# Performance work log

Measured on AMD Instinct MI355X. Metric: run time of the kernel, lower is better.

Reference implementation:

```python
import jax, jax.numpy as jnp
import numpy as np

EMB = 256
HEADS = 2
IMG = 224
P1, P2 = 16, 8
LN_EPS = 1e-5


def _layer_norm(t, g, b):
    m = jnp.mean(t, axis=-1, keepdims=True)
    v = jnp.mean((t - m) ** 2, axis=-1, keepdims=True)
    return (t - m) * jax.lax.rsqrt(v + LN_EPS) * g + b


def _patch_embed(x, W, b, cls_tok, p):
    B, C, H, Wd = x.shape
    h, w = H // p, Wd // p
    # b c (h p1)(w p2) -> b (h w) (p1 p2 c)
    t = x.reshape(B, C, h, p, w, p).transpose(0, 2, 4, 3, 5, 1).reshape(B, h * w, p * p * C)
    t = t @ W + b
    cls = jnp.broadcast_to(cls_tok, (B, 1, cls_tok.shape[-1]))
    return jnp.concatenate([cls, t], axis=1)


def setup_inputs() -> dict:
    key = jax.random.key(0)
    ks = jax.random.split(key, 16)
    s = 0.02
    d = {
        "x": jax.random.normal(ks[0], (128, 3, IMG, IMG), dtype=jnp.float32),
        "W1": jax.random.normal(ks[1], (P1 * P1 * 3, EMB), dtype=jnp.float32) * s,
        "b1": jnp.zeros((EMB,), jnp.float32),
        "cls1": jax.random.normal(ks[2], (1, 1, EMB), dtype=jnp.float32),
        "W2": jax.random.normal(ks[3], (P2 * P2 * 3, EMB), dtype=jnp.float32) * s,
        "b2": jnp.zeros((EMB,), jnp.float32),
        "cls2": jax.random.normal(ks[4], (1, 1, EMB), dtype=jnp.float32),
        "ln1_g": jnp.ones((EMB,), jnp.float32),
        "ln1_b": jnp.zeros((EMB,), jnp.float32),
        "Wq": jax.random.normal(ks[5], (EMB, EMB), dtype=jnp.float32) * s,
        "bq": jnp.zeros((EMB,), jnp.float32),
        "Wk": jax.random.normal(ks[6], (EMB, EMB), dtype=jnp.float32) * s,
        "bk": jnp.zeros((EMB,), jnp.float32),
        "Wv": jax.random.normal(ks[7], (EMB, EMB), dtype=jnp.float32) * s,
        "bv": jnp.zeros((EMB,), jnp.float32),
        "Wp": jax.random.normal(ks[8], (EMB, EMB), dtype=jnp.float32) * s,
        "bp": jnp.zeros((EMB,), jnp.float32),
        "ln2_g": jnp.ones((EMB,), jnp.float32),
        "ln2_b": jnp.zeros((EMB,), jnp.float32),
        "lnc_g": jnp.ones((EMB,), jnp.float32),
        "lnc_b": jnp.zeros((EMB,), jnp.float32),
        "Wc": jax.random.normal(ks[9], (EMB, 2), dtype=jnp.float32) * s,
        "bc": jnp.zeros((2,), jnp.float32),
    }
    return d


def reference(x, W1, b1, cls1, W2, b2, cls2, ln1_g, ln1_b, Wq, bq, Wk, bk, Wv, bv,
              Wp, bp, ln2_g, ln2_b, lnc_g, lnc_b, Wc, bc):
    B = x.shape[0]
    p1 = _patch_embed(x, W1, b1, cls1, P1)   # [B, 197, 256]
    p2 = _patch_embed(x, W2, b2, cls2, P2)   # [B, 785, 256]
    n = p1.shape[1]
    idx = jnp.linspace(0.0, p2.shape[1] - 1, n).astype(jnp.int32)  # truncation like .long()
    p2r = p2[:, idx, :]
    z = jnp.concatenate([p2r, p1], axis=1)   # [B, 394, 256]
    N = z.shape[1]

    h = _layer_norm(z, ln1_g, ln1_b)
    dh = EMB // HEADS
    q = (h @ Wq + bq).reshape(B, N, HEADS, dh).transpose(0, 2, 1, 3)
    k = (h @ Wk + bk).reshape(B, N, HEADS, dh).transpose(0, 2, 1, 3)
    v = (h @ Wv + bv).reshape(B, N, HEADS, dh).transpose(0, 2, 1, 3)
    attn = jnp.einsum('bhqd,bhkd->bhqk', q, k)
    # NOTE: faithful to source — softmax of UNscaled logits, then divide by sqrt(emb)
    attn = jax.nn.softmax(attn, axis=-1) / (EMB ** 0.5)
    o = jnp.einsum('bhqk,bhkd->bhqd', attn, v).transpose(0, 2, 1, 3).reshape(B, N, EMB)
    o = o @ Wp + bp
    o = _layer_norm(o, ln2_g, ln2_b)
    z = z + o

    pooled = jnp.mean(z, axis=1)
    logits = _layer_norm(pooled, lnc_g, lnc_b) @ Wc + bc
    return jax.nn.log_softmax(logits, axis=1)
```

## Files before the change

kernel.cpp:

```cpp
#include <hip/hip_runtime.h>

typedef short short8 __attribute__((ext_vector_type(8)));
typedef float f32x4 __attribute__((ext_vector_type(4)));
typedef unsigned short us4 __attribute__((ext_vector_type(4)));
typedef unsigned short u16;

#define MFMA(a,b,c) __builtin_amdgcn_mfma_f32_16x16x32_bf16((a),(b),(c),0,0,0)

__device__ __forceinline__ u16 f2b(float f) {
    union { float f; unsigned int i; } v; v.f = f;
    unsigned int x = v.i;
    return (u16)((x + 0x7fffu + ((x >> 16) & 1u)) >> 16);
}

__device__ __forceinline__ unsigned int pk2(float lo, float hi) {
    return (unsigned int)f2b(lo) | ((unsigned int)f2b(hi) << 16);
}

__global__ __launch_bounds__(256) void k_wtrans(const float* __restrict__ W1,
        const float* __restrict__ W2, const float* __restrict__ Wq, const float* __restrict__ Wk,
        const float* __restrict__ Wv, const float* __restrict__ Wp,
        u16* __restrict__ w1t, u16* __restrict__ w2t, u16* __restrict__ wqt,
        u16* __restrict__ wkt, u16* __restrict__ wvt, u16* __restrict__ wpt) {
    int bx = blockIdx.x, n = threadIdx.x;
    if (bx < 768) {
        int k = bx, c = k % 3, t = k / 3, pj = t & 15, pi = t >> 4;
        int kp2 = c*256 + pi*16 + pj;
        w1t[(size_t)(kp2 >> 5)*8192 + n*32 + (kp2 & 31)] = f2b(W1[(size_t)k*256 + n]);
    } else if (bx < 960) {
        int k = bx - 768, c = k % 3, t = k / 3, pj = t & 7, pi = t >> 3;
        int kp2 = c*64 + pi*8 + pj;
        w2t[(size_t)(kp2 >> 5)*8192 + n*32 + (kp2 & 31)] = f2b(W2[(size_t)k*256 + n]);
    } else if (bx < 1216) { int k = bx - 960;  wqt[(size_t)(k>>5)*8192 + n*32 + (k&31)] = f2b(Wq[(size_t)k*256 + n]); }
    else if (bx < 1472)   { int k = bx - 1216; wkt[(size_t)(k>>5)*8192 + n*32 + (k&31)] = f2b(Wk[(size_t)k*256 + n]); }
    else if (bx < 1728)   { int k = bx - 1472; wvt[(size_t)(k>>5)*8192 + n*32 + (k&31)] = f2b(Wv[(size_t)k*256 + n]); }
    else                  { int k = bx - 1728; wpt[(size_t)(k>>5)*8192 + n*32 + (k&31)] = f2b(Wp[(size_t)k*256 + n]); }
}

__global__ __launch_bounds__(256) void k_cls(const float* __restrict__ cls1,
        const float* __restrict__ cls2, const float* __restrict__ g1, const float* __restrict__ be1,
        float* __restrict__ z, u16* __restrict__ h) {
    __shared__ float red[16];
    int b = blockIdx.x, e = threadIdx.x, lane = e & 63, w = e >> 6;
    float v0 = cls2[e], v1 = cls1[e];
    z[((size_t)b*394 + 0)*256 + e]   = v0;
    z[((size_t)b*394 + 197)*256 + e] = v1;
    float s0 = v0, q0 = v0*v0, s1 = v1, q1 = v1*v1;
    #pragma unroll
    for (int m = 1; m < 64; m <<= 1) {
        s0 += __shfl_xor(s0, m); q0 += __shfl_xor(q0, m);
        s1 += __shfl_xor(s1, m); q1 += __shfl_xor(q1, m);
    }
    if (lane == 0) { red[w] = s0; red[4+w] = q0; red[8+w] = s1; red[12+w] = q1; }
    __syncthreads();
    float S0 = red[0]+red[1]+red[2]+red[3],   Q0 = red[4]+red[5]+red[6]+red[7];
    float S1 = red[8]+red[9]+red[10]+red[11], Q1 = red[12]+red[13]+red[14]+red[15];
    float m0 = S0*(1.f/256.f), r0 = rsqrtf(Q0*(1.f/256.f) - m0*m0 + 1e-5f);
    float m1 = S1*(1.f/256.f), r1 = rsqrtf(Q1*(1.f/256.f) - m1*m1 + 1e-5f);
    h[((size_t)b*394 + 0)*256 + e]   = f2b((v0-m0)*r0*g1[e] + be1[e]);
    h[((size_t)b*394 + 197)*256 + e] = f2b((v1-m1)*r1*g1[e] + be1[e]);
}

__global__ __launch_bounds__(256) void k_embed1(const float* __restrict__ x,
        const u16* __restrict__ w1t, const float* __restrict__ b1,
        const float* __restrict__ g1, const float* __restrict__ be1,
        float* __restrict__ z, u16* __restrict__ h) {
    __shared__ __align__(16) u16 A[16*776];
    __shared__ __align__(16) u16 Wst[8192];
    __shared__ __align__(16) float S[16*260];
    int b = blockIdx.y, g = blockIdx.x, tid = threadIdx.x;
    int p = tid >> 4, pi = tid & 15;
    int j = g*16 + p;
    uint4 wr0 = *(const uint4*)&w1t[tid*8];
    uint4 wr1 = *(const uint4*)&w1t[2048 + tid*8];
    uint4 wr2 = *(const uint4*)&w1t[4096 + tid*8];
    uint4 wr3 = *(const uint4*)&w1t[6144 + tid*8];
    auto stage = [&](const u16* base, int chunk) {
        __syncthreads();
        *(uint4*)&Wst[tid*8] = wr0;
        *(uint4*)&Wst[2048 + tid*8] = wr1;
        *(uint4*)&Wst[4096 + tid*8] = wr2;
        *(uint4*)&Wst[6144 + tid*8] = wr3;
        __syncthreads();
        if (base) {
            const u16* src = base + (size_t)chunk*8192;
            wr0 = *(const uint4*)&src[tid*8];
            wr1 = *(const uint4*)&src[2048 + tid*8];
            wr2 = *(const uint4*)&src[4096 + tid*8];
            wr3 = *(const uint4*)&src[6144 + tid*8];
        }
    };
    if (j < 196) {
        int hi = j / 14, wi = j - hi*14;
        #pragma unroll
        for (int c = 0; c < 3; ++c) {
            const float* src = x + (((size_t)b*3 + c)*224 + hi*16 + pi)*224 + wi*16;
            #pragma unroll
            for (int s4 = 0; s4 < 4; ++s4) {
                f32x4 r = *(const f32x4*)(src + s4*4);
                us4 o; o[0] = f2b(r[0]); o[1] = f2b(r[1]); o[2] = f2b(r[2]); o[3] = f2b(r[3]);
                *(us4*)&A[p*776 + c*256 + pi*16 + s4*4] = o;
            }
        }
    } else {
        us4 zer = {0,0,0,0};
        #pragma unroll
        for (int c = 0; c < 3; ++c)
            #pragma unroll
            for (int s4 = 0; s4 < 4; ++s4)
                *(us4*)&A[p*776 + c*256 + pi*16 + s4*4] = zer;
    }
    int w = tid >> 6, lane = tid & 63, quad = lane >> 4, tf = lane & 15;
    f32x4 zero = {0.f,0.f,0.f,0.f};
    f32x4 acc[4] = {zero,zero,zero,zero};
    #pragma unroll
    for (int ks = 0; ks < 24; ++ks) {
        stage(ks < 23 ? w1t : nullptr, ks + 1);
        short8 a = *(const short8*)&A[tf*776 + ks*32 + quad*8];
        #pragma unroll
        for (int nf = 0; nf < 4; ++nf) {
            short8 bb = *(const short8*)&Wst[(w*64 + nf*16 + tf)*32 + quad*8];
            acc[nf] = MFMA(a, bb, acc[nf]);
        }
    }
    #pragma unroll
    for (int nf = 0; nf < 4; ++nf) {
        int n = w*64 + nf*16 + tf;
        float bias = b1[n];
        #pragma unroll
        for (int i = 0; i < 4; ++i)
            S[(quad*4 + i)*260 + n] = acc[nf][i] + bias;
    }
    __syncthreads();
    #pragma unroll
    for (int rr = 0; rr < 4; ++rr) {
        int row = w*4 + rr;
        int j2 = g*16 + row;
        f32x4 v = *(const f32x4*)&S[row*260 + lane*4];
        float s = v[0]+v[1]+v[2]+v[3];
        float sq = v[0]*v[0]+v[1]*v[1]+v[2]*v[2]+v[3]*v[3];
        #pragma unroll
        for (int m = 1; m < 64; m <<= 1) { s += __shfl_xor(s, m); sq += __shfl_xor(sq, m); }
        float mean = s*(1.f/256.f);
        float rs = rsqrtf(sq*(1.f/256.f) - mean*mean + 1e-5f);
        if (j2 < 196) {
            size_t base = ((size_t)b*394 + 198 + j2)*256 + lane*4;
            *(f32x4*)&z[base] = v;
            us4 ho;
            #pragma unroll
            for (int c = 0; c < 4; ++c) {
                int e = lane*4 + c;
                ho[c] = f2b((v[c]-mean)*rs*g1[e] + be1[e]);
            }
            *(us4*)&h[base] = ho;
        }
    }
}

__global__ __launch_bounds__(256) void k_embed2(const float* __restrict__ x,
        const u16* __restrict__ w2t, const float* __restrict__ b2,
        const float* __restrict__ g1, const float* __restrict__ be1,
        float* __restrict__ z, u16* __restrict__ h) {
    __shared__ __align__(16) u16 A[16*200];
    __shared__ __align__(16) u16 Wst[8192];
    __shared__ __align__(16) float S[16*260];
    int b = blockIdx.y, g = blockIdx.x, tid = threadIdx.x;
    int p = tid >> 4, s16 = tid & 15;
    int pi = s16 >> 1, ph = s16 & 1;
    int it = g*16 + p + 1;
    uint4 wr0 = *(const uint4*)&w2t[tid*8];
    uint4 wr1 = *(const uint4*)&w2t[2048 + tid*8];
    uint4 wr2 = *(const uint4*)&w2t[4096 + tid*8];
    uint4 wr3 = *(const uint4*)&w2t[6144 + tid*8];
    auto stage = [&](const u16* base, int chunk) {
        __syncthreads();
        *(uint4*)&Wst[tid*8] = wr0;
        *(uint4*)&Wst[2048 + tid*8] = wr1;
        *(uint4*)&Wst[4096 + tid*8] = wr2;
        *(uint4*)&Wst[6144 + tid*8] = wr3;
        __syncthreads();
        if (base) {
            const u16* src = base + (size_t)chunk*8192;
            wr0 = *(const uint4*)&src[tid*8];
            wr1 = *(const uint4*)&src[2048 + tid*8];
            wr2 = *(const uint4*)&src[4096 + tid*8];
            wr3 = *(const uint4*)&src[6144 + tid*8];
        }
    };
    if (it <= 196) {
        int patch = 4*it - 1;
        int hi = patch / 28, wi = patch - hi*28;
        #pragma unroll
        for (int c = 0; c < 3; ++c) {
            const float* src = x + (((size_t)b*3 + c)*224 + hi*8 + pi)*224 + wi*8 + ph*4;
            f32x4 r = *(const f32x4*)src;
            us4 o; o[0] = f2b(r[0]); o[1] = f2b(r[1]); o[2] = f2b(r[2]); o[3] = f2b(r[3]);
            *(us4*)&A[p*200 + c*64 + pi*8 + ph*4] = o;
        }
    } else {
        us4 zer = {0,0,0,0};
        #pragma unroll
        for (int c = 0; c < 3; ++c)
            *(us4*)&A[p*200 + c*64 + pi*8 + ph*4] = zer;
    }
    int w = tid >> 6, lane = tid & 63, quad = lane >> 4, tf = lane & 15;
    f32x4 zero = {0.f,0.f,0.f,0.f};
    f32x4 acc[4] = {zero,zero,zero,zero};
    #pragma unroll
    for (int ks = 0; ks < 6; ++ks) {
        stage(ks < 5 ? w2t : nullptr, ks + 1);
        short8 a = *(const short8*)&A[tf*200 + ks*32 + quad*8];
        #pragma unroll
        for (int nf = 0; nf < 4; ++nf) {
            short8 bb = *(const short8*)&Wst[(w*64 + nf*16 + tf)*32 + quad*8];
            acc[nf] = MFMA(a, bb, acc[nf]);
        }
    }
    #pragma unroll
    for (int nf = 0; nf < 4; ++nf) {
        int n = w*64 + nf*16 + tf;
        float bias = b2[n];
        #pragma unroll
        for (int i = 0; i < 4; ++i)
            S[(quad*4 + i)*260 + n] = acc[nf][i] + bias;
    }
    __syncthreads();
    #pragma unroll
    for (int rr = 0; rr < 4; ++rr) {
        int row = w*4 + rr;
        int it2 = g*16 + row + 1;
        f32x4 v = *(const f32x4*)&S[row*260 + lane*4];
        float s = v[0]+v[1]+v[2]+v[3];
        float sq = v[0]*v[0]+v[1]*v[1]+v[2]*v[2]+v[3]*v[3];
        #pragma unroll
        for (int m = 1; m < 64; m <<= 1) { s += __shfl_xor(s, m); sq += __shfl_xor(sq, m); }
        float mean = s*(1.f/256.f);
        float rs = rsqrtf(sq*(1.f/256.f) - mean*mean + 1e-5f);
        if (it2 <= 196) {
            size_t base = ((size_t)b*394 + it2)*256 + lane*4;
            *(f32x4*)&z[base] = v;
            us4 ho;
            #pragma unroll
            for (int c = 0; c < 4; ++c) {
                int e = lane*4 + c;
                ho[c] = f2b((v[c]-mean)*rs*g1[e] + be1[e]);
            }
            *(us4*)&h[base] = ho;
        }
    }
}

__device__ __forceinline__ void store_qk(f32x4 acc[4][4], const float* __restrict__ bs,
        u16* __restrict__ dst, u16* Sst, int b, int mt, int w, int quad, int tf, int tid) {
    #pragma unroll
    for (int m = 0; m < 4; ++m) {
        __syncthreads();
        #pragma unroll
        for (int nf = 0; nf < 4; ++nf) {
            int e = w*64 + nf*16 + tf;
            float bias = bs[e];
            #pragma unroll
            for (int i = 0; i < 4; ++i) {
                int n = mt*64 + m*16 + quad*4 + i;
                Sst[(quad*4 + i)*264 + e] = (n < 394) ? f2b(acc[m][nf][i] + bias) : (u16)0;
            }
        }
        __syncthreads();
        int row = tid >> 4, c16 = tid & 15;
        int n = mt*64 + m*16 + row;
        if (n < 416) {
            int e0 = c16*16, hh = e0 >> 7, d0 = e0 & 127;
            uint4 v0 = *(const uint4*)&Sst[row*264 + e0];
            uint4 v1 = *(const uint4*)&Sst[row*264 + e0 + 8];
            u16* p = dst + ((size_t)(b*2 + hh)*416 + n)*128 + d0;
            *(uint4*)p = v0;
            *(uint4*)(p + 8) = v1;
        }
    }
}

__device__ __forceinline__ void store_v(f32x4 acc[4][4], const float* __restrict__ bs,
        u16* __restrict__ vt, u16* Sst, int b, int mt, int w, int quad, int tf, int tid) {
    #pragma unroll
    for (int nf = 0; nf < 4; ++nf) {
        __syncthreads();
        #pragma unroll
        for (int i = 0; i < 4; ++i) {
            int e = w*64 + nf*16 + quad*4 + i;
            float bias = bs[e];
            #pragma unroll
            for (int m = 0; m < 4; ++m) {
                int n = mt*64 + m*16 + tf;
                Sst[(w*16 + quad*4 + i)*72 + m*16 + tf] = (n < 394) ? f2b(acc[m][nf][i] + bias) : (u16)0;
            }
        }
        __syncthreads();
        #pragma unroll
        for (int k = 0; k < 2; ++k) {
            int ch = tid + k*256;
            int row = ch >> 3, c8 = ch & 7;
            int n0 = mt*64 + c8*8;
            if (n0 < 416) {
                int e = (row >> 4)*64 + nf*16 + (row & 15);
                int d = e & 127, hh = e >> 7;
                uint4 v = *(const uint4*)&Sst[row*72 + c8*8];
                *(uint4*)&vt[((size_t)(b*2 + hh)*128 + d)*416 + n0] = v;
            }
        }
    }
}

__global__ __launch_bounds__(256) void k_qkv(const u16* __restrict__ h,
        const u16* __restrict__ wqt, const u16* __restrict__ wkt, const u16* __restrict__ wvt,
        const float* __restrict__ bq, const float* __restrict__ bk, const float* __restrict__ bv,
        u16* __restrict__ q, u16* __restrict__ kb, u16* __restrict__ vt) {
    __shared__ __align__(16) u16 A[64*264];
    __shared__ __align__(16) u16 Wst[8192];
    __shared__ __align__(16) u16 Sst[4608];
    int mt = blockIdx.x, b = blockIdx.y, tid = threadIdx.x;
    uint4 wr0 = *(const uint4*)&wqt[tid*8];
    uint4 wr1 = *(const uint4*)&wqt[2048 + tid*8];
    uint4 wr2 = *(const uint4*)&wqt[4096 + tid*8];
    uint4 wr3 = *(const uint4*)&wqt[6144 + tid*8];
    auto stage = [&](const u16* base, int chunk) {
        __syncthreads();
        *(uint4*)&Wst[tid*8] = wr0;
        *(uint4*)&Wst[2048 + tid*8] = wr1;
        *(uint4*)&Wst[4096 + tid*8] = wr2;
        *(uint4*)&Wst[6144 + tid*8] = wr3;
        __syncthreads();
        if (base) {
            const u16* src = base + (size_t)chunk*8192;
            wr0 = *(const uint4*)&src[tid*8];
            wr1 = *(const uint4*)&src[2048 + tid*8];
            wr2 = *(const uint4*)&src[4096 + tid*8];
            wr3 = *(const uint4*)&src[6144 + tid*8];
        }
    };
    #pragma unroll
    for (int it = 0; it < 8; ++it) {
        int idx = tid + it*256;
        int row = idx >> 5, seg = idx & 31;
        int n = mt*64 + row;
        uint4 val = {0,0,0,0};
        if (n < 394) val = *(const uint4*)&h[((size_t)b*394 + n)*256 + seg*8];
        *(uint4*)&A[row*264 + seg*8] = val;
    }
    int w = tid >> 6, lane = tid & 63, quad = lane >> 4, tf = lane & 15;
    f32x4 zero = {0.f,0.f,0.f,0.f};

    {
        f32x4 acc[4][4];
        #pragma unroll
        for (int m = 0; m < 4; ++m)
            #pragma unroll
            for (int nf = 0; nf < 4; ++nf) acc[m][nf] = zero;
        #pragma unroll
        for (int ks = 0; ks < 8; ++ks) {
            stage(ks < 7 ? wqt : wkt, (ks + 1) & 7);
            short8 a0 = *(const short8*)&A[tf*264 + ks*32 + quad*8];
            short8 a1 = *(const short8*)&A[(16+tf)*264 + ks*32 + quad*8];
            short8 a2 = *(const short8*)&A[(32+tf)*264 + ks*32 + quad*8];
            short8 a3 = *(const short8*)&A[(48+tf)*264 + ks*32 + quad*8];
            #pragma unroll
            for (int nf = 0; nf < 4; ++nf) {
                short8 bb = *(const short8*)&Wst[(w*64 + nf*16 + tf)*32 + quad*8];
                acc[0][nf] = MFMA(a0, bb, acc[0][nf]);
                acc[1][nf] = MFMA(a1, bb, acc[1][nf]);
                acc[2][nf] = MFMA(a2, bb, acc[2][nf]);
                acc[3][nf] = MFMA(a3, bb, acc[3][nf]);
            }
        }
        store_qk(acc, bq, q, Sst, b, mt, w, quad, tf, tid);
    }
    {
        f32x4 acc[4][4];
        #pragma unroll
        for (int m = 0; m < 4; ++m)
            #pragma unroll
            for (int nf = 0; nf < 4; ++nf) acc[m][nf] = zero;
        #pragma unroll
        for (int ks = 0; ks < 8; ++ks) {
            stage(ks < 7 ? wkt : wvt, (ks + 1) & 7);
            short8 a0 = *(const short8*)&A[tf*264 + ks*32 + quad*8];
            short8 a1 = *(const short8*)&A[(16+tf)*264 + ks*32 + quad*8];
            short8 a2 = *(const short8*)&A[(32+tf)*264 + ks*32 + quad*8];
            short8 a3 = *(const short8*)&A[(48+tf)*264 + ks*32 + quad*8];
            #pragma unroll
            for (int nf = 0; nf < 4; ++nf) {
                short8 bb = *(const short8*)&Wst[(w*64 + nf*16 + tf)*32 + quad*8];
                acc[0][nf] = MFMA(a0, bb, acc[0][nf]);
                acc[1][nf] = MFMA(a1, bb, acc[1][nf]);
                acc[2][nf] = MFMA(a2, bb, acc[2][nf]);
                acc[3][nf] = MFMA(a3, bb, acc[3][nf]);
            }
        }
        store_qk(acc, bk, kb, Sst, b, mt, w, quad, tf, tid);
    }
    {
        f32x4 acc[4][4];
        #pragma unroll
        for (int m = 0; m < 4; ++m)
            #pragma unroll
            for (int nf = 0; nf < 4; ++nf) acc[m][nf] = zero;
        #pragma unroll
        for (int ks = 0; ks < 8; ++ks) {
            stage(ks < 7 ? wvt : nullptr, (ks + 1) & 7);
            short8 a0 = *(const short8*)&A[tf*264 + ks*32 + quad*8];
            short8 a1 = *(const short8*)&A[(16+tf)*264 + ks*32 + quad*8];
            short8 a2 = *(const short8*)&A[(32+tf)*264 + ks*32 + quad*8];
            short8 a3 = *(const short8*)&A[(48+tf)*264 + ks*32 + quad*8];
            #pragma unroll
            for (int nf = 0; nf < 4; ++nf) {
                short8 bb = *(const short8*)&Wst[(w*64 + nf*16 + tf)*32 + quad*8];
                acc[0][nf] = MFMA(bb, a0, acc[0][nf]);
                acc[1][nf] = MFMA(bb, a1, acc[1][nf]);
                acc[2][nf] = MFMA(bb, a2, acc[2][nf]);
                acc[3][nf] = MFMA(bb, a3, acc[3][nf]);
            }
        }
        store_v(acc, bv, vt, Sst, b, mt, w, quad, tf, tid);
    }
}

__global__ __launch_bounds__(256) void k_att(const u16* __restrict__ q,
        const u16* __restrict__ kbuf, const u16* __restrict__ vt, u16* __restrict__ o) {
    __shared__ __align__(16) u16 pool[9472];
    u16* Kst = pool;
    u16* Vst = pool + 4352;
    int nwg = gridDim.x * gridDim.y;
    int orig = blockIdx.y * gridDim.x + blockIdx.x;
    int q8 = nwg >> 3, r8 = nwg & 7;
    int xcd = orig & 7, idx = orig >> 3;
    int nid = (xcd < r8 ? xcd*(q8+1) : r8*(q8+1) + (xcd-r8)*q8) + idx;
    int bx = nid % 7, bh = nid / 7;
    int tid = threadIdx.x;
    int w = tid >> 6, lane = tid & 63, quad = lane >> 4, tf = lane & 15;
    int mt_raw = bx*4 + w;
    int mt = mt_raw < 26 ? mt_raw : 25;
    const u16* qp = q    + (size_t)bh*53248;
    const u16* kp = kbuf + (size_t)bh*53248;
    const u16* vp = vt   + (size_t)bh*53248;
    short8 afr[4];
    #pragma unroll
    for (int ks = 0; ks < 4; ++ks)
        afr[ks] = *(const short8*)&qp[(size_t)(mt*16 + tf)*128 + ks*32 + quad*8];
    f32x4 zero = {0.f,0.f,0.f,0.f};
    f32x4 acc[25];
    #pragma unroll
    for (int nt = 0; nt < 25; ++nt) acc[nt] = zero;
    int sr0 = tid >> 4, sseg = tid & 15;
    uint4 kreg0 = *(const uint4*)&kp[(size_t)sr0*128 + sseg*8];
    uint4 kreg1 = *(const uint4*)&kp[(size_t)(sr0+16)*128 + sseg*8];
    for (int kc = 0; kc < 13; ++kc) {
        __syncthreads();
        *(uint4*)&Kst[sr0*136 + sseg*8] = kreg0;
        *(uint4*)&Kst[(sr0+16)*136 + sseg*8] = kreg1;
        __syncthreads();
        if (kc < 12) {
            kreg0 = *(const uint4*)&kp[(size_t)((kc+1)*32 + sr0)*128 + sseg*8];
            kreg1 = *(const uint4*)&kp[(size_t)((kc+1)*32 + sr0 + 16)*128 + sseg*8];
        }
        #pragma unroll
        for (int ncl = 0; ncl < 2; ++ncl) {
            int nt = kc*2 + ncl;
            if (nt < 25) {
                #pragma unroll
                for (int ks = 0; ks < 4; ++ks) {
                    short8 kk = *(const short8*)&Kst[(ncl*16 + tf)*136 + ks*32 + quad*8];
                    acc[nt] = MFMA(kk, afr[ks], acc[nt]);
                }
            }
        }
    }
    int vd0 = tid >> 2, vseg = tid & 3;
    uint4 vreg0 = *(const uint4*)&vp[(size_t)vd0*416 + vseg*8];
    uint4 vreg1 = *(const uint4*)&vp[(size_t)(vd0+64)*416 + vseg*8];
    float mx = -3e38f;
    #pragma unroll
    for (int nt = 0; nt < 24; ++nt)
        #pragma unroll
        for (int i = 0; i < 4; ++i) mx = fmaxf(mx, acc[nt][i]);
    #pragma unroll
    for (int i = 0; i < 4; ++i)
        if (quad*4 + i < 10) mx = fmaxf(mx, acc[24][i]);
    mx = fmaxf(mx, __shfl_xor(mx, 16));
    mx = fmaxf(mx, __shfl_xor(mx, 32));
    float s = 0.f;
    #pragma unroll
    for (int nt = 0; nt < 24; ++nt)
        #pragma unroll
        for (int i = 0; i < 4; ++i) {
            float e = __expf(acc[nt][i] - mx);
            acc[nt][i] = e; s += e;
        }
    #pragma unroll
    for (int i = 0; i < 4; ++i) {
        if (quad*4 + i < 10) { float e = __expf(acc[24][i] - mx); acc[24][i] = e; s += e; }
        else acc[24][i] = 0.f;
    }
    s += __shfl_xor(s, 16);
    s += __shfl_xor(s, 32);
    float inv = 1.f / (16.f * s);
    #pragma unroll
    for (int nt = 0; nt < 25; ++nt)
        #pragma unroll
        for (int i = 0; i < 4; ++i) acc[nt][i] *= inv;
    f32x4 acc2[8];
    #pragma unroll
    for (int nf = 0; nf < 8; ++nf) acc2[nf] = zero;
    int qb0 = quad & 1;
    int g = (qb0 << 1) | (quad >> 1);
    for (int kc = 0; kc < 13; ++kc) {
        __syncthreads();
        *(uint4*)&Vst[vd0*40 + vseg*8] = vreg0;
        *(uint4*)&Vst[(vd0+64)*40 + vseg*8] = vreg1;
        __syncthreads();
        if (kc < 12) {
            vreg0 = *(const uint4*)&vp[(size_t)vd0*416 + (kc+1)*32 + vseg*8];
            vreg1 = *(const uint4*)&vp[(size_t)(vd0+64)*416 + (kc+1)*32 + vseg*8];
        }
        f32x4 v0 = acc[2*kc];
        f32x4 v1 = (kc < 12) ? acc[2*kc + 1] : zero;
        unsigned int r0 = pk2(v0[0], v0[1]);
        unsigned int r1 = pk2(v0[2], v0[3]);
        unsigned int r2 = pk2(v1[0], v1[1]);
        unsigned int r3 = pk2(v1[2], v1[3]);
        unsigned int sa = qb0 ? r0 : r2, sb = qb0 ? r1 : r3;
        unsigned int ra = (unsigned int)__shfl_xor((int)sa, 16);
        unsigned int rb = (unsigned int)__shfl_xor((int)sb, 16);
        unsigned int ka = qb0 ? r2 : r0, kb2 = qb0 ? r3 : r1;
        union { unsigned int u[4]; short8 s8; } au;
        au.u[0] = qb0 ? ra : ka;
        au.u[1] = qb0 ? rb : kb2;
        au.u[2] = qb0 ? ka : ra;
        au.u[3] = qb0 ? kb2 : rb;
        short8 a = au.s8;
        #pragma unroll
        for (int nf = 0; nf < 8; ++nf) {
            short8 bb = *(const short8*)&Vst[(nf*16 + tf)*40 + g*8];
            acc2[nf] = MFMA(a, bb, acc2[nf]);
        }
    }
    int b = bh >> 1, hh = bh & 1;
    __syncthreads();
    #pragma unroll
    for (int nf = 0; nf < 8; ++nf)
        #pragma unroll
        for (int i = 0; i < 4; ++i)
            pool[w*2176 + (quad*4 + i)*136 + nf*16 + tf] = f2b(acc2[nf][i]);
    __syncthreads();
    if (mt_raw < 26) {
        #pragma unroll
        for (int r4 = 0; r4 < 4; ++r4) {
            int rr = r4*4 + (lane >> 4);
            int n = mt_raw*16 + rr;
            if (n < 394) {
                int c16 = lane & 15;
                uint4 v = *(const uint4*)&pool[w*2176 + rr*136 + c16*8];
                *(uint4*)&o[((size_t)b*394 + n)*256 + hh*128 + c16*8] = v;
            }
        }
    }
}

__global__ __launch_bounds__(256) void k_proj(const u16* __restrict__ o,
        const u16* __restrict__ wpt, const float* __restrict__ bp,
        const float* __restrict__ g2, const float* __restrict__ bb2,
        float* __restrict__ z) {
    __shared__ __align__(16) u16 A[32*264];
    __shared__ __align__(16) u16 Wst[8192];
    __shared__ __align__(16) float S[32*260];
    int mt = blockIdx.x, b = blockIdx.y, tid = threadIdx.x;
    int w = tid >> 6, lane = tid & 63, quad = lane >> 4, tf = lane & 15;
    uint4 wr0 = *(const uint4*)&wpt[tid*8];
    uint4 wr1 = *(const uint4*)&wpt[2048 + tid*8];
    uint4 wr2 = *(const uint4*)&wpt[4096 + tid*8];
    uint4 wr3 = *(const uint4*)&wpt[6144 + tid*8];
    auto stage = [&](const u16* base, int chunk) {
        __syncthreads();
        *(uint4*)&Wst[tid*8] = wr0;
        *(uint4*)&Wst[2048 + tid*8] = wr1;
        *(uint4*)&Wst[4096 + tid*8] = wr2;
        *(uint4*)&Wst[6144 + tid*8] = wr3;
        __syncthreads();
        if (base) {
            const u16* src = base + (size_t)chunk*8192;
            wr0 = *(const uint4*)&src[tid*8];
            wr1 = *(const uint4*)&src[2048 + tid*8];
            wr2 = *(const uint4*)&src[4096 + tid*8];
            wr3 = *(const uint4*)&src[6144 + tid*8];
        }
    };
    for (int idx = tid; idx < 2048; idx += 256) {
        int row = idx >> 6, col4 = (idx & 63) * 4;
        int n = mt*32 + row;
        us4 val = {0,0,0,0};
        if (n < 394) val = *(const us4*)&o[((size_t)b*394 + n)*256 + col4];
        *(us4*)&A[row*264 + col4] = val;
    }
    f32x4 zero = {0.f,0.f,0.f,0.f};
    f32x4 acc[2][4];
    #pragma unroll
    for (int m = 0; m < 2; ++m)
        #pragma unroll
        for (int nf = 0; nf < 4; ++nf) acc[m][nf] = zero;
    #pragma unroll
    for (int ks = 0; ks < 8; ++ks) {
        stage(ks < 7 ? wpt : nullptr, ks + 1);
        short8 a0 = *(const short8*)&A[tf*264 + ks*32 + quad*8];
        short8 a1 = *(const short8*)&A[(16+tf)*264 + ks*32 + quad*8];
        #pragma unroll
        for (int nf = 0; nf < 4; ++nf) {
            short8 bb = *(const short8*)&Wst[(w*64 + nf*16 + tf)*32 + quad*8];
            acc[0][nf] = MFMA(a0, bb, acc[0][nf]);
            acc[1][nf] = MFMA(a1, bb, acc[1][nf]);
        }
    }
    #pragma unroll
    for (int nf = 0; nf < 4; ++nf) {
        int e = w*64 + nf*16 + tf;
        float bsv = bp[e];
        #pragma unroll
        for (int m = 0; m < 2; ++m)
            #pragma unroll
            for (int i = 0; i < 4; ++i)
                S[(m*16 + quad*4 + i)*260 + e] = acc[m][nf][i] + bsv;
    }
    __syncthreads();
    #pragma unroll
    for (int rr = 0; rr < 8; ++rr) {
        int row = w*8 + rr;
        f32x4 v = *(const f32x4*)&S[row*260 + lane*4];
        float s = v[0]+v[1]+v[2]+v[3];
        float sq = v[0]*v[0]+v[1]*v[1]+v[2]*v[2]+v[3]*v[3];
        #pragma unroll
        for (int m = 1; m < 64; m <<= 1) { s += __shfl_xor(s, m); sq += __shfl_xor(sq, m); }
        float mean = s*(1.f/256.f);
        float rs = rsqrtf(sq*(1.f/256.f) - mean*mean + 1e-5f);
        int n = mt*32 + row;
        if (n < 394) {
            float* zr = z + ((size_t)b*394 + n)*256 + lane*4;
            f32x4 zv = *(f32x4*)zr;
            #pragma unroll
            for (int c = 0; c < 4; ++c) {
                int e = lane*4 + c;
                zv[c] += (v[c]-mean)*rs*g2[e] + bb2[e];
            }
            *(f32x4*)zr = zv;
        }
    }
}

__global__ __launch_bounds__(256) void k_pool(const float* __restrict__ z,
        const float* __restrict__ lg, const float* __restrict__ lb,
        const float* __restrict__ wc, const float* __restrict__ bc,
        float* __restrict__ out) {
    __shared__ float red[8];
    int b = blockIdx.x, e = threadIdx.x;
    int wave = e >> 6, lane = e & 63;
    const float* zp = z + (size_t)b*394*256 + e;
    float p0 = 0.f, p1 = 0.f, p2 = 0.f, p3 = 0.f;
    int n = 0;
    for (; n + 3 < 394; n += 4) {
        p0 += zp[(size_t)n*256];       p1 += zp[(size_t)(n+1)*256];
        p2 += zp[(size_t)(n+2)*256];   p3 += zp[(size_t)(n+3)*256];
    }
    for (; n < 394; ++n) p0 += zp[(size_t)n*256];
    float pooled = (p0+p1+p2+p3) * (1.f/394.f);
    float a = pooled, sq = pooled*pooled;
    #pragma unroll
    for (int m = 1; m < 64; m <<= 1) { a += __shfl_xor(a, m); sq += __shfl_xor(sq, m); }
    if (lane == 0) { red[wave] = a; red[4+wave] = sq; }
    __syncthreads();
    float tot = red[0]+red[1]+red[2]+red[3];
    float totq = red[4]+red[5]+red[6]+red[7];
    float mean = tot*(1.f/256.f);
    float rs = rsqrtf(totq*(1.f/256.f) - mean*mean + 1e-5f);
    float ln = (pooled-mean)*rs*lg[e] + lb[e];
    float t0 = ln * wc[e*2], t1 = ln * wc[e*2+1];
    #pragma unroll
    for (int m = 1; m < 64; m <<= 1) { t0 += __shfl_xor(t0, m); t1 += __shfl_xor(t1, m); }
    __syncthreads();
    if (lane == 0) { red[wave] = t0; red[4+wave] = t1; }
    __syncthreads();
    if (e < 2) {
        float l0 = red[0]+red[1]+red[2]+red[3] + bc[0];
        float l1 = red[4]+red[5]+red[6]+red[7] + bc[1];
        float mx = fmaxf(l0, l1);
        float lse = mx + logf(__expf(l0-mx) + __expf(l1-mx));
        out[b*2 + e] = (e == 0 ? l0 : l1) - lse;
    }
}

extern "C" void kernel_launch(void* const* d_in, const int* in_sizes, int n_in,
                              void* d_out, int out_size, void* d_ws, size_t ws_size,
                              hipStream_t stream) {
    const float* x    = (const float*)d_in[0];
    const float* W1   = (const float*)d_in[1];
    const float* b1   = (const float*)d_in[2];
    const float* cls1 = (const float*)d_in[3];
    const float* W2   = (const float*)d_in[4];
    const float* b2   = (const float*)d_in[5];
    const float* cls2 = (const float*)d_in[6];
    const float* ln1g = (const float*)d_in[7];
    const float* ln1b = (const float*)d_in[8];
    const float* Wq   = (const float*)d_in[9];
    const float* bq   = (const float*)d_in[10];
    const float* Wk   = (const float*)d_in[11];
    const float* bk   = (const float*)d_in[12];
    const float* Wv   = (const float*)d_in[13];
    const float* bv   = (const float*)d_in[14];
    const float* Wp   = (const float*)d_in[15];
    const float* bp   = (const float*)d_in[16];
    const float* ln2g = (const float*)d_in[17];
    const float* ln2b = (const float*)d_in[18];
    const float* lncg = (const float*)d_in[19];
    const float* lncb = (const float*)d_in[20];
    const float* Wc   = (const float*)d_in[21];
    const float* bcp  = (const float*)d_in[22];

    int Bn = in_sizes[0] / (3*224*224);

    const size_t WBYTES = 1015808;
    const size_t PER_IMG = 403456 + 201728 + 212992*3;
    size_t avail = (ws_size > WBYTES) ? ws_size - WBYTES : 0;
    int Bc = (int)(avail / PER_IMG);
    if (Bc < 1) Bc = 1;
    if (Bc > Bn) Bc = Bn;

    u16* w1t = (u16*)d_ws;
    u16* w2t = w1t + 196608;
    u16* wqt = w2t + 49152;
    u16* wkt = wqt + 65536;
    u16* wvt = wkt + 65536;
    u16* wpt = wvt + 65536;
    float* z = (float*)(wpt + 65536);
    u16* h   = (u16*)(z + (size_t)Bc*100864);
    u16* o   = h;
    u16* q   = h + (size_t)Bc*100864;
    u16* kb  = q + (size_t)Bc*106496;
    u16* vt  = kb + (size_t)Bc*106496;

    k_wtrans<<<1984, 256, 0, stream>>>(W1, W2, Wq, Wk, Wv, Wp, w1t, w2t, wqt, wkt, wvt, wpt);

    for (int b0 = 0; b0 < Bn; b0 += Bc) {
        int bc = (Bn - b0 < Bc) ? (Bn - b0) : Bc;
        const float* xb = x + (size_t)b0 * 3*224*224;
        float* outb = (float*)d_out + (size_t)b0 * 2;

        k_cls<<<bc, 256, 0, stream>>>(cls1, cls2, ln1g, ln1b, z, h);
        k_embed1<<<dim3(13, bc), 256, 0, stream>>>(xb, w1t, b1, ln1g, ln1b, z, h);
        k_embed2<<<dim3(13, bc), 256, 0, stream>>>(xb, w2t, b2, ln1g, ln1b, z, h);
        k_qkv<<<dim3(7, bc), 256, 0, stream>>>(h, wqt, wkt, wvt, bq, bk, bv, q, kb, vt);
        k_att<<<dim3(7, bc*2), 256, 0, stream>>>(q, kb, vt, o);
        k_proj<<<dim3(13, bc), 256, 0, stream>>>(o, wpt, bp, ln2g, ln2b, z);
        k_pool<<<bc, 256, 0, stream>>>(z, lncg, lncb, Wc, bcp, outb);
    }
}
```

Baseline: 395.0 us.

## Split patch-embed-1 into im2col pass and 64-row tiled MFMA GEMM with fused LN

The 16x16 patch embedding is split into two kernels. The first converts image patches to a bf16 im2col matrix in scratch memory (reusing the q/k buffers). The second is a GEMM that tiles 64 rows per block with double-buffered LDS for both A and weights, so each weight chunk is reused across four times as many rows. LayerNorm statistics are now reduced directly from the accumulators instead of through an fp32 staging tile. In exchange, the im2col matrix makes an extra round trip through global memory and adds a kernel launch.

```diff
diff --git a/kernel.cpp b/kernel.cpp
--- a/kernel.cpp
+++ b/kernel.cpp
@@ -61,100 +61,144 @@
     h[((size_t)b*394 + 197)*256 + e] = f2b((v1-m1)*r1*g1[e] + be1[e]);
 }
 
-__global__ __launch_bounds__(256) void k_embed1(const float* __restrict__ x,
-        const u16* __restrict__ w1t, const float* __restrict__ b1,
-        const float* __restrict__ g1, const float* __restrict__ be1,
-        float* __restrict__ z, u16* __restrict__ h) {
-    __shared__ __align__(16) u16 A[16*776];
-    __shared__ __align__(16) u16 Wst[8192];
-    __shared__ __align__(16) float S[16*260];
+__global__ __launch_bounds__(256) void k_im2col1(const float* __restrict__ x,
+        u16* __restrict__ A1) {
     int b = blockIdx.y, g = blockIdx.x, tid = threadIdx.x;
     int p = tid >> 4, pi = tid & 15;
     int j = g*16 + p;
-    uint4 wr0 = *(const uint4*)&w1t[tid*8];
-    uint4 wr1 = *(const uint4*)&w1t[2048 + tid*8];
-    uint4 wr2 = *(const uint4*)&w1t[4096 + tid*8];
-    uint4 wr3 = *(const uint4*)&w1t[6144 + tid*8];
-    auto stage = [&](const u16* base, int chunk) {
-        __syncthreads();
-        *(uint4*)&Wst[tid*8] = wr0;
-        *(uint4*)&Wst[2048 + tid*8] = wr1;
-        *(uint4*)&Wst[4096 + tid*8] = wr2;
-        *(uint4*)&Wst[6144 + tid*8] = wr3;
-        __syncthreads();
-        if (base) {
-            const u16* src = base + (size_t)chunk*8192;
-            wr0 = *(const uint4*)&src[tid*8];
-            wr1 = *(const uint4*)&src[2048 + tid*8];
-            wr2 = *(const uint4*)&src[4096 + tid*8];
-            wr3 = *(const uint4*)&src[6144 + tid*8];
-        }
-    };
+    u16* dst = A1 + ((size_t)b*208 + j)*768;
     if (j < 196) {
         int hi = j / 14, wi = j - hi*14;
         #pragma unroll
         for (int c = 0; c < 3; ++c) {
             const float* src = x + (((size_t)b*3 + c)*224 + hi*16 + pi)*224 + wi*16;
-            #pragma unroll
-            for (int s4 = 0; s4 < 4; ++s4) {
-                f32x4 r = *(const f32x4*)(src + s4*4);
-                us4 o; o[0] = f2b(r[0]); o[1] = f2b(r[1]); o[2] = f2b(r[2]); o[3] = f2b(r[3]);
-                *(us4*)&A[p*776 + c*256 + pi*16 + s4*4] = o;
-            }
+            f32x4 r0 = *(const f32x4*)(src);
+            f32x4 r1 = *(const f32x4*)(src + 4);
+            f32x4 r2 = *(const f32x4*)(src + 8);
+            f32x4 r3 = *(const f32x4*)(src + 12);
+            union { u16 u[16]; uint4 q[2]; } t;
+            #pragma unroll
+            for (int s = 0; s < 4; ++s) {
+                t.u[s] = f2b(r0[s]); t.u[4+s] = f2b(r1[s]);
+                t.u[8+s] = f2b(r2[s]); t.u[12+s] = f2b(r3[s]);
+            }
+            *(uint4*)&dst[c*256 + pi*16] = t.q[0];
+            *(uint4*)&dst[c*256 + pi*16 + 8] = t.q[1];
         }
     } else {
-        us4 zer = {0,0,0,0};
-        #pragma unroll
-        for (int c = 0; c < 3; ++c)
-            #pragma unroll
-            for (int s4 = 0; s4 < 4; ++s4)
-                *(us4*)&A[p*776 + c*256 + pi*16 + s4*4] = zer;
-    }
+        uint4 zer = {0,0,0,0};
+        #pragma unroll
+        for (int c = 0; c < 3; ++c) {
+            *(uint4*)&dst[c*256 + pi*16] = zer;
+            *(uint4*)&dst[c*256 + pi*16 + 8] = zer;
+        }
+    }
+}
+
+__global__ __launch_bounds__(256) void k_embed1(const u16* __restrict__ A1,
+        const u16* __restrict__ w1t, const float* __restrict__ b1,
+        const float* __restrict__ g1, const float* __restrict__ be1,
+        float* __restrict__ z, u16* __restrict__ h, int nrows) {
+    __shared__ __align__(16) u16 Ab[2][64*40];
+    __shared__ __align__(16) u16 Bb[2][256*40];
+    __shared__ float red[64][8];
+    int tid = threadIdx.x;
+    int r0 = blockIdx.x * 64;
     int w = tid >> 6, lane = tid & 63, quad = lane >> 4, tf = lane & 15;
+    int arow = tid >> 2, aoff = (tid & 3) * 8;
+    const u16* ap = A1 + (size_t)(r0 + arow)*768 + aoff;
+    uint4 ra  = *(const uint4*)(ap);
+    uint4 rb0 = *(const uint4*)&w1t[tid*8];
+    uint4 rb1 = *(const uint4*)&w1t[2048 + tid*8];
+    uint4 rb2 = *(const uint4*)&w1t[4096 + tid*8];
+    uint4 rb3 = *(const uint4*)&w1t[6144 + tid*8];
     f32x4 zero = {0.f,0.f,0.f,0.f};
-    f32x4 acc[4] = {zero,zero,zero,zero};
-    #pragma unroll
-    for (int ks = 0; ks < 24; ++ks) {
-        stage(ks < 23 ? w1t : nullptr, ks + 1);
-        short8 a = *(const short8*)&A[tf*776 + ks*32 + quad*8];
+    f32x4 acc[4][4];
+    #pragma unroll
+    for (int m = 0; m < 4; ++m)
+        #pragma unroll
+        for (int nf = 0; nf < 4; ++nf) acc[m][nf] = zero;
+    #pragma unroll
+    for (int kc = 0; kc < 24; ++kc) {
+        int buf = kc & 1;
+        *(uint4*)&Ab[buf][arow*40 + aoff] = ra;
+        *(uint4*)&Bb[buf][(arow      )*40 + aoff] = rb0;
+        *(uint4*)&Bb[buf][(arow +  64)*40 + aoff] = rb1;
+        *(uint4*)&Bb[buf][(arow + 128)*40 + aoff] = rb2;
+        *(uint4*)&Bb[buf][(arow + 192)*40 + aoff] = rb3;
+        int nc = kc < 23 ? kc + 1 : 23;
+        ra = *(const uint4*)(ap + nc*32);
+        const u16* src = w1t + (size_t)nc*8192;
+        rb0 = *(const uint4*)&src[tid*8];
+        rb1 = *(const uint4*)&src[2048 + tid*8];
+        rb2 = *(const uint4*)&src[4096 + tid*8];
+        rb3 = *(const uint4*)&src[6144 + tid*8];
+        __syncthreads();
+        short8 a0 = *(const short8*)&Ab[buf][(     tf)*40 + quad*8];
+        short8 a1 = *(const short8*)&Ab[buf][(16 + tf)*40 + quad*8];
+        short8 a2 = *(const short8*)&Ab[buf][(32 + tf)*40 + quad*8];
+        short8 a3 = *(const short8*)&Ab[buf][(48 + tf)*40 + quad*8];
         #pragma unroll
         for (int nf = 0; nf < 4; ++nf) {
-            short8 bb = *(const short8*)&Wst[(w*64 + nf*16 + tf)*32 + quad*8];
-            acc[nf] = MFMA(a, bb, acc[nf]);
-        }
-    }
+            short8 bb = *(const short8*)&Bb[buf][(w*64 + nf*16 + tf)*40 + quad*8];
+            acc[0][nf] = MFMA(a0, bb, acc[0][nf]);
+            acc[1][nf] = MFMA(a1, bb, acc[1][nf]);
+            acc[2][nf] = MFMA(a2, bb, acc[2][nf]);
+            acc[3][nf] = MFMA(a3, bb, acc[3][nf]);
+        }
+    }
+    float bias[4], gv[4], bev[4];
     #pragma unroll
     for (int nf = 0; nf < 4; ++nf) {
         int n = w*64 + nf*16 + tf;
-        float bias = b1[n];
-        #pragma unroll
-        for (int i = 0; i < 4; ++i)
-            S[(quad*4 + i)*260 + n] = acc[nf][i] + bias;
-    }
+        bias[nf] = b1[n]; gv[nf] = g1[n]; bev[nf] = be1[n];
+    }
+    #pragma unroll
+    for (int m = 0; m < 4; ++m)
+        #pragma unroll
+        for (int nf = 0; nf < 4; ++nf)
+            #pragma unroll
+            for (int i = 0; i < 4; ++i) acc[m][nf][i] += bias[nf];
+    #pragma unroll
+    for (int m = 0; m < 4; ++m)
+        #pragma unroll
+        for (int i = 0; i < 4; ++i) {
+            float s = acc[m][0][i] + acc[m][1][i] + acc[m][2][i] + acc[m][3][i];
+            float qv = acc[m][0][i]*acc[m][0][i] + acc[m][1][i]*acc[m][1][i]
+                     + acc[m][2][i]*acc[m][2][i] + acc[m][3][i]*acc[m][3][i];
+            #pragma unroll
+            for (int d = 1; d < 16; d <<= 1) { s += __shfl_xor(s, d); qv += __shfl_xor(qv, d); }
+            if (tf == 0) {
+                red[m*16 + quad*4 + i][w] = s;
+                red[m*16 + quad*4 + i][4 + w] = qv;
+            }
+        }
     __syncthreads();
     #pragma unroll
-    for (int rr = 0; rr < 4; ++rr) {
-        int row = w*4 + rr;
-        int j2 = g*16 + row;
-        f32x4 v = *(const f32x4*)&S[row*260 + lane*4];
-        float s = v[0]+v[1]+v[2]+v[3];
-        float sq = v[0]*v[0]+v[1]*v[1]+v[2]*v[2]+v[3]*v[3];
-        #pragma unroll
-        for (int m = 1; m < 64; m <<= 1) { s += __shfl_xor(s, m); sq += __shfl_xor(sq, m); }
-        float mean = s*(1.f/256.f);
-        float rs = rsqrtf(sq*(1.f/256.f) - mean*mean + 1e-5f);
-        if (j2 < 196) {
-            size_t base = ((size_t)b*394 + 198 + j2)*256 + lane*4;
-            *(f32x4*)&z[base] = v;
-            us4 ho;
-            #pragma unroll
-            for (int c = 0; c < 4; ++c) {
-                int e = lane*4 + c;
-                ho[c] = f2b((v[c]-mean)*rs*g1[e] + be1[e]);
-            }
-            *(us4*)&h[base] = ho;
-        }
-    }
+    for (int m = 0; m < 4; ++m)
+        #pragma unroll
+        for (int i = 0; i < 4; ++i) {
+            int rl = m*16 + quad*4 + i;
+            float S = red[rl][0]+red[rl][1]+red[rl][2]+red[rl][3];
+            float Q = red[rl][4]+red[rl][5]+red[rl][6]+red[rl][7];
+            float mean = S*(1.f/256.f);
+            float rs = rsqrtf(Q*(1.f/256.f) - mean*mean + 1e-5f);
+            int row = r0 + rl;
+            if (row < nrows) {
+                int img = row / 208;
+                int j = row - img*208;
+                if (j < 196) {
+                    size_t base = ((size_t)img*394 + 198 + j)*256;
+                    #pragma unroll
+                    for (int nf = 0; nf < 4; ++nf) {
+                        int n = w*64 + nf*16 + tf;
+                        float v = acc[m][nf][i];
+                        z[base + n] = v;
+                        h[base + n] = f2b((v - mean)*rs*gv[nf] + bev[nf]);
+                    }
+                }
+            }
+        }
 }
 
 __global__ __launch_bounds__(256) void k_embed2(const float* __restrict__ x,
@@ -748,9 +792,12 @@
         int bc = (Bn - b0 < Bc) ? (Bn - b0) : Bc;
         const float* xb = x + (size_t)b0 * 3*224*224;
         float* outb = (float*)d_out + (size_t)b0 * 2;
+        int nrows = bc * 208;
+        int gm = (nrows + 63) / 64;
 
         k_cls<<<bc, 256, 0, stream>>>(cls1, cls2, ln1g, ln1b, z, h);
-        k_embed1<<<dim3(13, bc), 256, 0, stream>>>(xb, w1t, b1, ln1g, ln1b, z, h);
+        k_im2col1<<<dim3(13, bc), 256, 0, stream>>>(xb, q );
+        k_embed1<<<gm, 256, 0, stream>>>(q , w1t, b1, ln1g, ln1b, z, h, nrows);
         k_embed2<<<dim3(13, bc), 256, 0, stream>>>(xb, w2t, b2, ln1g, ln1b, z, h);
         k_qkv<<<dim3(7, bc), 256, 0, stream>>>(h, wqt, wkt, wvt, bq, bk, bv, q, kb, vt);
         k_att<<<dim3(7, bc*2), 256, 0, stream>>>(q, kb, vt, o);
```

After: 391.2 us. About the same (-1.0%).
